# Kernel optimization log

Measured on AMD Instinct MI355X. Metric: run time of the kernel, lower is better.

The kernel has to match this reference:

```python
import jax, jax.numpy as jnp
import numpy as np

DIM = 1024
HEADS = 16
HEAD_DIM = DIM // HEADS
K = 13              # kernel_size (odd)
NS = K // 2         # neighborhood radius
SCALE = HEAD_DIM ** -0.5


def setup_inputs() -> dict:
    key = jax.random.key(0)
    ks = jax.random.split(key, 5)
    B, L = 2, 4096
    x = jax.random.normal(ks[0], (B, L, DIM), jnp.float32)
    qkv_w = jax.random.normal(ks[1], (3 * DIM, DIM), jnp.float32) * 0.02
    qkv_b = jnp.zeros((3 * DIM,), jnp.float32)
    rpb = jax.random.normal(ks[2], (HEADS, 2 * K - 1), jnp.float32) * 0.02  # trunc_normal std=0.02
    proj_w = jax.random.normal(ks[3], (DIM, DIM), jnp.float32) * 0.02
    proj_b = jnp.zeros((DIM,), jnp.float32)
    return dict(x=x, qkv_w=qkv_w, qkv_b=qkv_b, rpb=rpb, proj_w=proj_w, proj_b=proj_b)


def reference(x, qkv_w, qkv_b, rpb, proj_w, proj_b):
    B, L, C = x.shape
    # qkv projection (torch Linear convention: y = x @ W^T + b)
    qkv = (x @ qkv_w.T + qkv_b).reshape(B, L, 3, HEADS, HEAD_DIM).transpose(2, 0, 3, 1, 4)
    q, k, v = qkv[0] * SCALE, qkv[1], qkv[2]  # each [B, H, L, D]

    i = jnp.arange(L)
    # NATTEN 1D window start (dilation=1): clamp window fully inside [0, L)
    ni = jnp.clip(i - NS, 0, L - K)                       # [L]
    # relative-position-bias start index per query (NATTEN get_pb_start)
    pi = NS + jnp.where(i < NS, NS - i, 0) + jnp.where(i + NS >= L, L - i - 1 - NS, 0)  # [L]
    j = jnp.arange(K)
    nbr = ni[:, None] + j[None, :]                        # [L, K] neighbor key indices
    bidx = pi[:, None] + j[None, :]                       # [L, K] rpb indices in [0, 2K-2]

    kg = k[:, :, nbr, :]                                  # [B, H, L, K, D]
    vg = v[:, :, nbr, :]                                  # [B, H, L, K, D]

    attn = jnp.einsum('bhld,bhlkd->bhlk', q, kg) + rpb[:, bidx][None]  # [B, H, L, K]
    attn = jax.nn.softmax(attn, axis=-1)
    out = jnp.einsum('bhlk,bhlkd->bhld', attn, vg)        # [B, H, L, D]
    out = out.transpose(0, 2, 1, 3).reshape(B, L, C)
    return out @ proj_w.T + proj_b
```

## Files before the change

### kernel.cpp

```cpp
#include <hip/hip_runtime.h>
#include <hip/hip_bf16.h>

#define DIMC 1024
#define HEADS 16
#define HEAD_DIM 64
#define KWIN 13
#define NSH 6
#define LSEQ 4096
#define BATCH 2
#define NROWS (BATCH*LSEQ)
#define QKV_N (3*DIMC)
#define SCALE_Q 0.125f

#define TBLK 256
#define WROWS 268

typedef __attribute__((ext_vector_type(4))) float f32x4;
typedef __attribute__((ext_vector_type(8))) short bf16x8;

__device__ __forceinline__ void gload_lds16(const void* g, void* l) {
  __builtin_amdgcn_global_load_lds(
      (const __attribute__((address_space(1))) void*)g,
      (__attribute__((address_space(3))) void*)l, 16, 0, 0);
}

__device__ __forceinline__ void cvt8(uint4 r, float* f) {
  unsigned u[4] = {r.x, r.y, r.z, r.w};
#pragma unroll
  for (int w = 0; w < 4; w++) {
    f[2*w]   = __uint_as_float(u[w] << 16);
    f[2*w+1] = __uint_as_float(u[w] & 0xffff0000u);
  }
}

__global__ __launch_bounds__(256) void cast3_kernel(const float* __restrict__ in0, __hip_bfloat16* __restrict__ out0, int n0,
                                                    const float* __restrict__ in1, __hip_bfloat16* __restrict__ out1, int n1,
                                                    const float* __restrict__ in2, __hip_bfloat16* __restrict__ out2, int n2) {
  int i = blockIdx.x * 256 + threadIdx.x;
  const float* in; __hip_bfloat16* out; int k;
  if (i < n0) { in = in0; out = out0; k = i; }
  else if (i < n0 + n1) { in = in1; out = out1; k = i - n0; }
  else if (i < n0 + n1 + n2) { in = in2; out = out2; k = i - n0 - n1; }
  else return;
  const float4* p = (const float4*)in + (size_t)k * 2;
  float4 a = p[0], b = p[1];
  union { ushort us[8]; uint4 v; } o;
  __hip_bfloat16 h;
  h = __float2bfloat16(a.x); o.us[0] = *(ushort*)&h;
  h = __float2bfloat16(a.y); o.us[1] = *(ushort*)&h;
  h = __float2bfloat16(a.z); o.us[2] = *(ushort*)&h;
  h = __float2bfloat16(a.w); o.us[3] = *(ushort*)&h;
  h = __float2bfloat16(b.x); o.us[4] = *(ushort*)&h;
  h = __float2bfloat16(b.y); o.us[5] = *(ushort*)&h;
  h = __float2bfloat16(b.z); o.us[6] = *(ushort*)&h;
  h = __float2bfloat16(b.w); o.us[7] = *(ushort*)&h;
  ((uint4*)out)[k] = o.v;
}


#define STAGE4(s) do { \
  __hip_bfloat16* dst_ = smem + (s) * 8192 + wave * 1024; \
  gload_lds16(gA,       dst_); \
  gload_lds16(gA + r16, dst_ + 512); \
  gload_lds16(gB,       dst_ + 4096); \
  gload_lds16(gB + r16, dst_ + 4096 + 512); \
} while (0)

#define COMPUTE16(s) do { \
  const __hip_bfloat16* As_ = smem + (s) * 8192; \
  const __hip_bfloat16* Bs_ = As_ + 4096; \
  bf16x8 af[4], bfr[4]; \
  _Pragma("unroll") for (int i = 0; i < 4; i++) \
    af[i] = *(const bf16x8*)&As_[(wr * 64 + i * 16 + fr) * 32 + fk0]; \
  _Pragma("unroll") for (int i = 0; i < 4; i++) \
    bfr[i] = *(const bf16x8*)&Bs_[(wc * 64 + i * 16 + fr) * 32 + fk0]; \
  _Pragma("unroll") for (int mi = 0; mi < 4; mi++) \
  _Pragma("unroll") for (int ni = 0; ni < 4; ni++) \
    acc[mi][ni] = __builtin_amdgcn_mfma_f32_16x16x32_bf16(af[mi], bfr[ni], acc[mi][ni], 0, 0, 0); \
} while (0)

template<int OUT_BF16>
__global__ __launch_bounds__(256) void gemm_bt(const __hip_bfloat16* __restrict__ A,
                                               const __hip_bfloat16* __restrict__ B,
                                               const float* __restrict__ bias,
                                               void* __restrict__ Cout,
                                               int M, int N, int K, int nbx) {
  __shared__ __align__(16) __hip_bfloat16 smem[16384];

  const int tid  = threadIdx.x;
  const int lane = tid & 63;
  const int wave = tid >> 6;

  int id = blockIdx.x;
  {
    const int nwg = gridDim.x;
    const int q = nwg >> 3, r = nwg & 7;
    const int xcd = id & 7, off = id >> 3;
    id = (xcd < r ? xcd * (q + 1) : r * (q + 1) + (xcd - r) * q) + off;
  }
  const int bx = id % nbx;
  const int by = id / nbx;
  const int m0 = by * 128;
  const int n0 = bx * 128;
  const int wr = wave >> 1;
  const int wc = wave & 1;

  f32x4 acc[4][4] = {};

  const int rA0  = wave * 32 + (lane >> 2);
  const int kcol = ((lane & 3) ^ ((lane >> 3) & 3)) * 8;
  const __hip_bfloat16* gA = A + (size_t)(m0 + rA0) * K + kcol;
  const __hip_bfloat16* gB = B + (size_t)(n0 + rA0) * K + kcol;
  const size_t r16 = (size_t)16 * K;

  const int fr  = lane & 15;
  const int fq  = lane >> 4;
  const int fk0 = ((fq ^ ((fr >> 1) & 3)) & 3) * 8;

  const int NT = K >> 5;

  STAGE4(0);
  gA += 32; gB += 32;
  __syncthreads();

  int cur = 0;
#pragma unroll 1
  for (int t = 1; t < NT; t++) {
    STAGE4(cur ^ 1);
    gA += 32; gB += 32;
    COMPUTE16(cur);
    __syncthreads();
    cur ^= 1;
  }
  COMPUTE16(cur);

#pragma unroll
  for (int ni = 0; ni < 4; ni++) {
    const int col = n0 + wc * 64 + ni * 16 + (lane & 15);
    const float bv = bias[col];
#pragma unroll
    for (int mi = 0; mi < 4; mi++) {
      const int row = m0 + wr * 64 + mi * 16 + ((lane >> 4) << 2);
#pragma unroll
      for (int i = 0; i < 4; i++) {
        const float v = acc[mi][ni][i] + bv;
        if (OUT_BF16)
          ((__hip_bfloat16*)Cout)[(size_t)(row + i) * N + col] = __float2bfloat16(v);
        else
          ((float*)Cout)[(size_t)(row + i) * N + col] = v;
      }
    }
  }
}

__global__ __launch_bounds__(256, 2) void natten(const __hip_bfloat16* __restrict__ qkv,
                                                 const float* __restrict__ rpb,
                                                 __hip_bfloat16* __restrict__ att) {
  __shared__ __align__(16) unsigned char smem[2 * WROWS * 128];

  const int tid = threadIdx.x;
  const int tb  = blockIdx.x;
  const int h   = blockIdx.y;
  const int b   = blockIdx.z;
  const int t0  = tb * TBLK;

  int r0 = t0 - NSH;
  if (r0 < 0) r0 = 0;
  if (r0 > LSEQ - WROWS) r0 = LSEQ - WROWS;

  const __hip_bfloat16* kg = qkv + ((size_t)b * LSEQ + r0) * QKV_N + DIMC + h * HEAD_DIM;
  const __hip_bfloat16* vg = kg + DIMC;
#pragma unroll 1
  for (int i = tid; i < WROWS * 8; i += 256) {
    const int row = i >> 3, c = i & 7;
    const uint4 kk = *(const uint4*)(kg + (size_t)row * QKV_N + c * 8);
    const uint4 vv = *(const uint4*)(vg + (size_t)row * QKV_N + c * 8);
    const int off = row * 128 + ((c * 16) ^ ((row & 7) << 4));
    *(uint4*)(smem + off) = kk;
    *(uint4*)(smem + WROWS * 128 + off) = vv;
  }
  __syncthreads();

  const int t = t0 + tid;
  int ni = t - NSH;
  ni = ni < 0 ? 0 : (ni > LSEQ - KWIN ? LSEQ - KWIN : ni);
  const int rbase = ni - r0;
  const int pi = NSH + (t < NSH ? NSH - t : 0) + (t + NSH >= LSEQ ? LSEQ - t - 1 - NSH : 0);
  const float* rp = rpb + h * (2 * KWIN - 1) + pi;

  const __hip_bfloat16* qg = qkv + ((size_t)b * LSEQ + t) * QKV_N + h * HEAD_DIM;
  float qf[64];
#pragma unroll
  for (int c = 0; c < 8; c++) {
    uint4 qq = *(const uint4*)(qg + c * 8);
    cvt8(qq, qf + c * 8);
  }

  float p[KWIN];
#pragma unroll
  for (int j = 0; j < KWIN; j++) {
    const int row = rbase + j;
    const int sw = (row & 7) << 4;
    float s = 0.f;
#pragma unroll
    for (int c = 0; c < 8; c++) {
      uint4 kk = *(const uint4*)(smem + row * 128 + ((c * 16) ^ sw));
      float kf[8];
      cvt8(kk, kf);
#pragma unroll
      for (int e = 0; e < 8; e++) s += qf[c * 8 + e] * kf[e];
    }
    p[j] = s * SCALE_Q + rp[j];
  }

  float m = p[0];
#pragma unroll
  for (int j = 1; j < KWIN; j++) m = fmaxf(m, p[j]);
  float sum = 0.f;
#pragma unroll
  for (int j = 0; j < KWIN; j++) { p[j] = __expf(p[j] - m); sum += p[j]; }
  const float inv = 1.f / sum;
#pragma unroll
  for (int j = 0; j < KWIN; j++) p[j] *= inv;

  __hip_bfloat16* og = att + ((size_t)b * LSEQ + t) * DIMC + h * HEAD_DIM;
#pragma unroll
  for (int c = 0; c < 8; c++) {
    float acc[8] = {0.f, 0.f, 0.f, 0.f, 0.f, 0.f, 0.f, 0.f};
#pragma unroll
    for (int j = 0; j < KWIN; j++) {
      const int row = rbase + j;
      uint4 vv = *(const uint4*)(smem + WROWS * 128 + row * 128 + ((c * 16) ^ ((row & 7) << 4)));
      float vf[8];
      cvt8(vv, vf);
#pragma unroll
      for (int e = 0; e < 8; e++) acc[e] += p[j] * vf[e];
    }
    union { ushort us[8]; uint4 v; } o;
#pragma unroll
    for (int e = 0; e < 8; e++) {
      __hip_bfloat16 hb = __float2bfloat16(acc[e]);
      o.us[e] = *(ushort*)&hb;
    }
    *(uint4*)(og + c * 8) = o.v;
  }
}

extern "C" void kernel_launch(void* const* d_in, const int* in_sizes, int n_in,
                              void* d_out, int out_size, void* d_ws, size_t ws_size,
                              hipStream_t stream) {
  const float* x      = (const float*)d_in[0];
  const float* qkv_w  = (const float*)d_in[1];
  const float* qkv_b  = (const float*)d_in[2];
  const float* rpb    = (const float*)d_in[3];
  const float* proj_w = (const float*)d_in[4];
  const float* proj_b = (const float*)d_in[5];
  float* out = (float*)d_out;

  char* ws = (char*)d_ws;
  __hip_bfloat16* xb    = (__hip_bfloat16*)(ws);
  __hip_bfloat16* wqkv  = (__hip_bfloat16*)(ws + 16777216);
  __hip_bfloat16* wproj = (__hip_bfloat16*)(ws + 23068672);
  __hip_bfloat16* qkv   = (__hip_bfloat16*)(ws + 25165824);
  __hip_bfloat16* att   = (__hip_bfloat16*)(ws + 75497472);

  const int n0 = NROWS * DIMC / 8;
  const int n1 = QKV_N * DIMC / 8;
  const int n2 = DIMC * DIMC / 8;
  cast3_kernel<<<(n0 + n1 + n2 + 255) / 256, 256, 0, stream>>>(
      x, xb, n0, qkv_w, wqkv, n1, proj_w, wproj, n2);

  gemm_bt<1><<<(QKV_N / 128) * (NROWS / 128), 256, 0, stream>>>(
      xb, wqkv, qkv_b, (void*)qkv, NROWS, QKV_N, DIMC, QKV_N / 128);

  natten<<<dim3(LSEQ / TBLK, HEADS, BATCH), 256, 0, stream>>>(qkv, rpb, att);

  gemm_bt<0><<<(DIMC / 128) * (NROWS / 128), 256, 0, stream>>>(
      att, wproj, proj_b, (void*)out, NROWS, DIMC, DIMC, DIMC / 128);
}
```

Measured before the change: 134.5 us.

## Load GEMM B operand directly into registers instead of staging through LDS

The B-matrix tile is no longer copied into shared memory; each wave loads its MFMA B fragments straight from global memory into double-buffered registers, while A still goes through LDS via global_load_lds. This halves LDS footprint and LDS read traffic and is meant to raise occupancy and cut LDS bandwidth pressure. In exchange, B rows are now loaded redundantly by the two waves sharing a column block, through uncoalesced strided 16-byte loads, and register pressure rises. The loop is unrolled by two with fixed buffer ping-pong, which assumes NT is even.

```diff
diff --git a/kernel.cpp b/kernel.cpp
--- a/kernel.cpp
+++ b/kernel.cpp
@@ -58,25 +58,27 @@
 }
 
 
-#define STAGE4(s) do { \
-  __hip_bfloat16* dst_ = smem + (s) * 8192 + wave * 1024; \
+#define STAGEA(s) do { \
+  __hip_bfloat16* dst_ = smem + (s) * 4096 + wave * 1024; \
   gload_lds16(gA,       dst_); \
   gload_lds16(gA + r16, dst_ + 512); \
-  gload_lds16(gB,       dst_ + 4096); \
-  gload_lds16(gB + r16, dst_ + 4096 + 512); \
+  gA += 32; \
 } while (0)
 
-#define COMPUTE16(s) do { \
-  const __hip_bfloat16* As_ = smem + (s) * 8192; \
-  const __hip_bfloat16* Bs_ = As_ + 4096; \
-  bf16x8 af[4], bfr[4]; \
+#define LOADB(dst, t) do { \
+  const __hip_bfloat16* p_ = gBr + (size_t)(t) * 32; \
+  _Pragma("unroll") for (int i = 0; i < 4; i++) \
+    dst[i] = *(const bf16x8*)(p_ + (size_t)i * 16 * K); \
+} while (0)
+
+#define COMPUTEAB(s, breg) do { \
+  const __hip_bfloat16* As_ = smem + (s) * 4096; \
+  bf16x8 af[4]; \
   _Pragma("unroll") for (int i = 0; i < 4; i++) \
     af[i] = *(const bf16x8*)&As_[(wr * 64 + i * 16 + fr) * 32 + fk0]; \
-  _Pragma("unroll") for (int i = 0; i < 4; i++) \
-    bfr[i] = *(const bf16x8*)&Bs_[(wc * 64 + i * 16 + fr) * 32 + fk0]; \
   _Pragma("unroll") for (int mi = 0; mi < 4; mi++) \
   _Pragma("unroll") for (int ni = 0; ni < 4; ni++) \
-    acc[mi][ni] = __builtin_amdgcn_mfma_f32_16x16x32_bf16(af[mi], bfr[ni], acc[mi][ni], 0, 0, 0); \
+    acc[mi][ni] = __builtin_amdgcn_mfma_f32_16x16x32_bf16(af[mi], breg[ni], acc[mi][ni], 0, 0, 0); \
 } while (0)
 
 template<int OUT_BF16>
@@ -85,7 +87,7 @@
                                                const float* __restrict__ bias,
                                                void* __restrict__ Cout,
                                                int M, int N, int K, int nbx) {
-  __shared__ __align__(16) __hip_bfloat16 smem[16384];
+  __shared__ __align__(16) __hip_bfloat16 smem[8192];
 
   const int tid  = threadIdx.x;
   const int lane = tid & 63;
@@ -110,29 +112,30 @@
   const int rA0  = wave * 32 + (lane >> 2);
   const int kcol = ((lane & 3) ^ ((lane >> 3) & 3)) * 8;
   const __hip_bfloat16* gA = A + (size_t)(m0 + rA0) * K + kcol;
-  const __hip_bfloat16* gB = B + (size_t)(n0 + rA0) * K + kcol;
   const size_t r16 = (size_t)16 * K;
 
   const int fr  = lane & 15;
   const int fq  = lane >> 4;
   const int fk0 = ((fq ^ ((fr >> 1) & 3)) & 3) * 8;
 
+  const __hip_bfloat16* gBr = B + (size_t)(n0 + wc * 64 + fr) * K + fq * 8;
+
+  bf16x8 b0[4], b1[4];
+
   const int NT = K >> 5;
 
-  STAGE4(0);
-  gA += 32; gB += 32;
+  STAGEA(0);
+  LOADB(b0, 0);
   __syncthreads();
 
-  int cur = 0;
+  int t = 1;
 #pragma unroll 1
-  for (int t = 1; t < NT; t++) {
-    STAGE4(cur ^ 1);
-    gA += 32; gB += 32;
-    COMPUTE16(cur);
-    __syncthreads();
-    cur ^= 1;
-  }
-  COMPUTE16(cur);
+  for (int i = 0; i < (NT - 2) / 2; i++) {
+    STAGEA(1); LOADB(b1, t); COMPUTEAB(0, b0); __syncthreads(); t++;
+    STAGEA(0); LOADB(b0, t); COMPUTEAB(1, b1); __syncthreads(); t++;
+  }
+  STAGEA(1); LOADB(b1, t); COMPUTEAB(0, b0); __syncthreads();
+  COMPUTEAB(1, b1);
 
 #pragma unroll
   for (int ni = 0; ni < 4; ni++) {
```

New measurement: 189.7 us. +41.0%, slower.
